# Performance work log

Measured on AMD Instinct MI355X. Metric: run time of the kernel, lower is better.

## Reference

```python
import jax, jax.numpy as jnp
import numpy as np

D_K = 128
D_V = 128
SEQ_LEN = 2048


def setup_inputs() -> dict:
    key = jax.random.key(0)
    kq, kk, kv = jax.random.split(key, 3)
    q = jax.random.normal(kq, (SEQ_LEN, D_K), dtype=jnp.float32)
    k = jax.random.normal(kk, (SEQ_LEN, D_K), dtype=jnp.float32)
    v = jax.random.normal(kv, (SEQ_LEN, D_V), dtype=jnp.float32)
    return {"q": q, "k": k, "v": v}


def _step(carry, qkv):
    J, Svv, Sqv, Sqq, l = carry
    q, k, v = qkv
    l = l + 1
    fl = l.astype(J.dtype)
    # update_correlations: running means of outer products
    Svv = (fl - 1.0) / fl * Svv + jnp.outer(v, v) / fl
    Sqv = (fl - 1.0) / fl * Sqv + jnp.outer(q, v) / fl
    Sqq = (fl - 1.0) / fl * Sqq + jnp.outer(q, q) / fl

    first = l == 1

    # ecological params (J: [d_v, d_k], Sqv: [d_k, d_v], Sqq: [d_k, d_k])
    s_J = jnp.einsum('vk,kv->', J, Sqv)            # trace(J @ Sigma_qv)
    s_l = k @ Sqv @ v
    A_JJ = jnp.einsum('vk,kj,vj->', J, Sqq, J)     # trace(J Sqq J^T)
    A_ll = (v @ v) * (k @ Sqq @ k)
    A_Jl = v @ J @ Sqq @ k

    # safe denominators (unused branches must not produce NaN under where)
    A_JJ_s = jnp.where(first | (A_JJ == 0), 1.0, A_JJ)
    A_ll_s = jnp.where(first | (A_ll == 0), 1.0, A_ll)
    denom = A_JJ * A_ll - A_Jl ** 2
    denom_s = jnp.where(first | (denom == 0), 1.0, denom)

    margin = s_l - A_Jl * (s_J / A_JJ_s)

    wf = (A_ll * s_J - A_Jl * s_l) / denom_s
    wi = (A_JJ * s_l - A_Jl * s_J) / denom_s
    # nonnegativity constraints (check omega_i first, as in the source)
    wf_c = jnp.where(wi <= 0, s_J / A_JJ_s, jnp.where(wf <= 0, 0.0, wf))
    wi_c = jnp.where(wi <= 0, 0.0, jnp.where(wf <= 0, s_l / A_ll_s, wi))

    do_update = margin > 0
    vk = jnp.outer(v, k)
    J_upd = jnp.where(do_update, wf_c * J + wi_c * vk, J)
    J_new = jnp.where(first, vk, J_upd)
    updated = first | do_update

    # compute_cost with updated J and correlations
    cost = (0.5 * jnp.trace(Svv)
            - jnp.einsum('vk,kv->', J_new, Sqv)
            + 0.5 * jnp.einsum('vk,kj,vj->', J_new, Sqq, J_new))

    return (J_new, Svv, Sqv, Sqq, l), (cost, updated)


def _run(q, k, v):
    d_k, d_v = q.shape[-1], v.shape[-1]
    init = (jnp.zeros((d_v, d_k), q.dtype),
            jnp.zeros((d_v, d_v), q.dtype),
            jnp.zeros((d_k, d_v), q.dtype),
            jnp.zeros((d_k, d_k), q.dtype),
            jnp.int32(0))
    (J, _, _, _, _), (costs, updated) = jax.lax.scan(_step, init, (q, k, v))
    return costs, updated, J


def reference(q, k, v):
    return _run(q, k, v)
```

## Files before the change

kernel.cpp:

```cpp
#include <hip/hip_runtime.h>

#define SEQ 2048
#define D 128

__global__ __launch_bounds__(256) void precompute_kernel(
    const float* __restrict__ q, const float* __restrict__ k, const float* __restrict__ v,
    float* __restrict__ U, float* __restrict__ sl, float* __restrict__ kqq,
    float* __restrict__ vv, float* __restrict__ kq_adj, float* __restrict__ vv_adj,
    float* __restrict__ kU_adj, double* __restrict__ invl)
{
    const int s = blockIdx.x;
    const int tid = threadIdx.x;

    __shared__ float ks[D];
    __shared__ float vs[D];
    __shared__ float alpha[SEQ];
    __shared__ float red[8];
    __shared__ float upart[256];

    if (tid < D) ks[tid] = k[s * D + tid];
    else if (tid < 2 * D) vs[tid - D] = v[s * D + (tid - D)];
    __syncthreads();

    float p_a2 = 0.f, p_ab = 0.f;
    for (int i = tid; i <= s; i += 256) {
        const float4* qr = (const float4*)(q + (size_t)i * D);
        const float4* vr = (const float4*)(v + (size_t)i * D);
        float a = 0.f, b = 0.f;
#pragma unroll
        for (int j = 0; j < D / 4; ++j) {
            float4 q4 = qr[j];
            float4 v4 = vr[j];
            a += q4.x * ks[4 * j + 0] + q4.y * ks[4 * j + 1] + q4.z * ks[4 * j + 2] + q4.w * ks[4 * j + 3];
            b += v4.x * vs[4 * j + 0] + v4.y * vs[4 * j + 1] + v4.z * vs[4 * j + 2] + v4.w * vs[4 * j + 3];
        }
        alpha[i] = a;
        p_a2 += a * a;
        p_ab += a * b;
        if (i == s) vv[s] = b;
    }
#pragma unroll
    for (int off = 1; off < 64; off <<= 1) {
        p_a2 += __shfl_xor(p_a2, off);
        p_ab += __shfl_xor(p_ab, off);
    }
    const int wid = tid >> 6;
    if ((tid & 63) == 0) { red[wid] = p_a2; red[4 + wid] = p_ab; }
    __syncthreads();
    if (tid == 0) {
        kqq[s] = red[0] + red[1] + red[2] + red[3];
        sl[s]  = red[4] + red[5] + red[6] + red[7];
        invl[s] = 1.0 / (double)(s + 1);
    }

    if (tid < 64) {
        if (s + 1 < SEQ) {
            float p2 = ks[tid] * q[(size_t)(s + 1) * D + tid]
                     + ks[tid + 64] * q[(size_t)(s + 1) * D + 64 + tid];
#pragma unroll
            for (int off = 1; off < 64; off <<= 1) p2 += __shfl_xor(p2, off);
            if (tid == 0) kq_adj[s + 1] = p2;
        }
        if (s == 0 && tid == 0) { kq_adj[0] = 0.f; kU_adj[0] = 0.f; vv_adj[0] = 0.f; }
    } else if (tid < 128 && s > 0) {
        const int t2 = tid - 64;
        float p2 = vs[t2] * v[(size_t)(s - 1) * D + t2]
                 + vs[t2 + 64] * v[(size_t)(s - 1) * D + 64 + t2];
#pragma unroll
        for (int off = 1; off < 64; off <<= 1) p2 += __shfl_xor(p2, off);
        if (t2 == 0) vv_adj[s] = p2;
    }

    const int c = tid & (D - 1);
    const int h = tid >> 7;
    float a0 = 0.f, a1 = 0.f, a2 = 0.f, a3 = 0.f;
    int i = h;
    for (; i + 6 <= s; i += 8) {
        a0 = fmaf(q[(size_t)(i    ) * D + c], alpha[i    ], a0);
        a1 = fmaf(q[(size_t)(i + 2) * D + c], alpha[i + 2], a1);
        a2 = fmaf(q[(size_t)(i + 4) * D + c], alpha[i + 4], a2);
        a3 = fmaf(q[(size_t)(i + 6) * D + c], alpha[i + 6], a3);
    }
    for (; i <= s; i += 2) a0 = fmaf(q[(size_t)i * D + c], alpha[i], a0);
    upart[tid] = (a0 + a1) + (a2 + a3);
    __syncthreads();

    float kup = 0.f;
    if (tid < D) {
        const float uv = upart[tid] + upart[tid + D];
        U[(size_t)s * D + tid] = uv;
        if (s > 0) kup = uv * k[(size_t)(s - 1) * D + tid];
    }
#pragma unroll
    for (int off = 1; off < 64; off <<= 1) kup += __shfl_xor(kup, off);
    if (tid == 0)  red[0] = kup;
    if (tid == 64) red[1] = kup;
    __syncthreads();
    if (s > 0 && tid == 0) kU_adj[s] = red[0] + red[1];
}

#define DPP_ADD(x, ctrl) \
    ((x) + __int_as_float(__builtin_amdgcn_update_dpp(0, __float_as_int(x), (ctrl), 0xf, 0xf, true)))
#define COMBINE8(x) do { x = DPP_ADD(x, 0xB1); x = DPP_ADD(x, 0x4E); x = DPP_ADD(x, 0x141); } while (0)
#define TAIL3(x)    do { x = DPP_ADD(x, 0x140); x = DPP_ADD(x, 0x142); x = DPP_ADD(x, 0x143); } while (0)
#define REDUCE16(x) do { x = DPP_ADD(x, 0xB1); x = DPP_ADD(x, 0x4E); x = DPP_ADD(x, 0x141); \
                         x = DPP_ADD(x, 0x140); } while (0)

#define UPDATE_J(MODE, WF, WI)                                                            \
    if ((MODE) == 2) {                                                                    \
        jr0.x = vcur*kk0.x; jr0.y = vcur*kk0.y; jr0.z = vcur*kk0.z; jr0.w = vcur*kk0.w;   \
        jr1.x = vcur*kk1.x; jr1.y = vcur*kk1.y; jr1.z = vcur*kk1.z; jr1.w = vcur*kk1.w;   \
        jr2.x = vcur*kk2.x; jr2.y = vcur*kk2.y; jr2.z = vcur*kk2.z; jr2.w = vcur*kk2.w;   \
        jr3.x = vcur*kk3.x; jr3.y = vcur*kk3.y; jr3.z = vcur*kk3.z; jr3.w = vcur*kk3.w;   \
    } else if ((MODE) == 1) {                                                             \
        const float wvr = (WI) * vcur;                                                    \
        jr0.x = fmaf(jr0.x, (WF), wvr*kk0.x); jr0.y = fmaf(jr0.y, (WF), wvr*kk0.y);       \
        jr0.z = fmaf(jr0.z, (WF), wvr*kk0.z); jr0.w = fmaf(jr0.w, (WF), wvr*kk0.w);       \
        jr1.x = fmaf(jr1.x, (WF), wvr*kk1.x); jr1.y = fmaf(jr1.y, (WF), wvr*kk1.y);       \
        jr1.z = fmaf(jr1.z, (WF), wvr*kk1.z); jr1.w = fmaf(jr1.w, (WF), wvr*kk1.w);       \
        jr2.x = fmaf(jr2.x, (WF), wvr*kk2.x); jr2.y = fmaf(jr2.y, (WF), wvr*kk2.y);       \
        jr2.z = fmaf(jr2.z, (WF), wvr*kk2.z); jr2.w = fmaf(jr2.w, (WF), wvr*kk2.w);       \
        jr3.x = fmaf(jr3.x, (WF), wvr*kk3.x); jr3.y = fmaf(jr3.y, (WF), wvr*kk3.y);       \
        jr3.z = fmaf(jr3.z, (WF), wvr*kk3.z); jr3.w = fmaf(jr3.w, (WF), wvr*kk3.w);       \
    }

__global__ __launch_bounds__(1024, 4) void scan_kernel(
    const float* __restrict__ q, const float* __restrict__ k, const float* __restrict__ v,
    const float* __restrict__ U, const float* __restrict__ sl_arr,
    const float* __restrict__ kqq_arr, const float* __restrict__ vv_arr,
    const float* __restrict__ kq_adj, const float* __restrict__ vv_adj,
    const float* __restrict__ kU_adj, const double* __restrict__ invl_arr,
    float* __restrict__ out)
{
    const int tid  = threadIdx.x;
    const int lane = tid & 63;
    const int w    = __builtin_amdgcn_readfirstlane(tid >> 6);
    const int r    = tid >> 3;
    const int cg   = tid & 7;
    const int c0s  = cg * 20;

    float4 jr0 = make_float4(0.f, 0.f, 0.f, 0.f);
    float4 jr1 = jr0, jr2 = jr0, jr3 = jr0;

    __shared__ float ring[3][3][160];
    __shared__ __align__(16) float wred[2][16][4];
    __shared__ __align__(16) float decLDS[2][4];

    const bool stager = (tid >= 384) && (tid < 768);
    const int  which  = (tid >> 7) - 3;
    const int  sidx   = tid & 127;
    const int  widx   = ((sidx >> 4) * 20) + (sidx & 15);

    float gstage = 0.f;
    if (stager) {
        if (which == 0) {
            ring[0][0][widx] = q[(size_t)1 * D + sidx];
            ring[1][0][widx] = q[(size_t)2 * D + sidx];
            gstage = q[(size_t)3 * D + sidx];
        } else if (which == 1) {
            ring[0][1][widx] = U[(size_t)1 * D + sidx];
            ring[1][1][widx] = U[(size_t)2 * D + sidx];
            gstage = U[(size_t)3 * D + sidx];
        } else {
            ring[0][2][widx] = k[sidx];
            ring[1][2][widx] = k[(size_t)1 * D + sidx];
            gstage = k[(size_t)2 * D + sidx];
        }
    }
    float vcur = v[r], vnext = v[(size_t)D + r], vn2 = v[(size_t)2 * D + r];

    float dwf = 0.f, dwi = 1.f;
    int dmode = 2;
    if (tid == 0) { decLDS[0][0] = 0.f; decLDS[0][1] = 1.f; decLDS[0][2] = 2.f; decLDS[0][3] = 0.f; }

    double SJ = 0.0, AJJ = 0.0, trSvv = 0.0;
    if (w == 0) {
        const double sl0 = (double)sl_arr[0];
        const double kq0 = (double)kqq_arr[0];
        const double vv0 = (double)vv_arr[0];
        trSvv = vv0;
        SJ  = sl0;
        AJJ = vv0 * kq0;
        if (lane == 0) {
            out[0] = (float)((0.5 * trSvv - SJ + 0.5 * AJJ) * invl_arr[0]);
            out[SEQ] = 1.f;
        }
    }
    __syncthreads();

    for (int i = 0; i < SEQ - 1; ++i) {
        const int p    = i % 3;
        const int pw   = (i + 2) % 3;
        const int par  = i & 1;
        const int parn = (i + 1) & 1;

        float c_sl = 0.f, c_kq = 0.f, c_vv = 0.f, c_kqa = 0.f, c_vva = 0.f,
              c_vvp = 0.f, c_kua = 0.f;
        double c_inv = 0.0;
        if (w == 0) {
            c_sl  = sl_arr[i + 1];  c_kq  = kqq_arr[i + 1]; c_vv  = vv_arr[i + 1];
            c_kqa = kq_adj[i + 1];  c_vva = vv_adj[i + 1];  c_vvp = vv_arr[i];
            c_kua = kU_adj[i + 1];  c_inv = invl_arr[i + 1];
        }

        const float4* q4 = (const float4*)&ring[p][0][c0s];
        const float4* u4 = (const float4*)&ring[p][1][c0s];
        const float4* k4 = (const float4*)&ring[p][2][c0s];
        const float4 qa = q4[0], qb = q4[1], qc = q4[2], qd = q4[3];
        const float4 ua = u4[0], ub = u4[1], uc = u4[2], ud = u4[3];
        const float4 kk0 = k4[0], kk1 = k4[1], kk2 = k4[2], kk3 = k4[3];

        float pa = jr0.x * qa.x, pb = jr2.x * qc.x;
        pa = fmaf(jr0.y, qa.y, pa); pb = fmaf(jr2.y, qc.y, pb);
        pa = fmaf(jr0.z, qa.z, pa); pb = fmaf(jr2.z, qc.z, pb);
        pa = fmaf(jr0.w, qa.w, pa); pb = fmaf(jr2.w, qc.w, pb);
        pa = fmaf(jr1.x, qb.x, pa); pb = fmaf(jr3.x, qd.x, pb);
        pa = fmaf(jr1.y, qb.y, pa); pb = fmaf(jr3.y, qd.y, pb);
        pa = fmaf(jr1.z, qb.z, pa); pb = fmaf(jr3.z, qd.z, pb);
        pa = fmaf(jr1.w, qb.w, pa); pb = fmaf(jr3.w, qd.w, pb);
        float Yq = pa + pb;
        float va_ = jr0.x * ua.x, vb_ = jr2.x * uc.x;
        va_ = fmaf(jr0.y, ua.y, va_); vb_ = fmaf(jr2.y, uc.y, vb_);
        va_ = fmaf(jr0.z, ua.z, va_); vb_ = fmaf(jr2.z, uc.z, vb_);
        va_ = fmaf(jr0.w, ua.w, va_); vb_ = fmaf(jr2.w, uc.w, vb_);
        va_ = fmaf(jr1.x, ub.x, va_); vb_ = fmaf(jr3.x, ud.x, vb_);
        va_ = fmaf(jr1.y, ub.y, va_); vb_ = fmaf(jr3.y, ud.y, vb_);
        va_ = fmaf(jr1.z, ub.z, va_); vb_ = fmaf(jr3.z, ud.z, vb_);
        va_ = fmaf(jr1.w, ub.w, va_); vb_ = fmaf(jr3.w, ud.w, vb_);
        float Yw = va_ + vb_;

        COMBINE8(Yq);
        COMBINE8(Yw);
        float z1 = vnext * Yq;
        float z2 = Yq * Yq;
        float z3 = vcur  * Yq;
        float z4 = vnext * Yw;
        TAIL3(z1);
        TAIL3(z2);
        TAIL3(z3);
        TAIL3(z4);
        if (lane == 63) *(float4*)&wred[par][w][0] = make_float4(z1, z2, z3, z4);

        if (stager) {
            ring[pw][which][widx] = gstage;
            const int tq = (i + 4 < SEQ) ? i + 4 : SEQ - 1;
            const int tk = (i + 3 < SEQ) ? i + 3 : SEQ - 1;
            gstage = (which == 0) ? q[(size_t)tq * D + sidx]
                   : (which == 1) ? U[(size_t)tq * D + sidx]
                                  : k[(size_t)tk * D + sidx];
        }
        const int tv = (i + 3 < SEQ) ? i + 3 : SEQ - 1;
        const float vnew = v[(size_t)tv * D + r];

        __syncthreads();

        if (w == 0) {
            float4 ww = *(const float4*)&wred[par][lane & 15][0];
            const float odwf = dwf, odwi = dwi;
            const int   odmode = dmode;
            UPDATE_J(odmode, odwf, odwi)

            REDUCE16(ww.x);
            REDUCE16(ww.y);
            REDUCE16(ww.z);
            REDUCE16(ww.w);

            double a, b;
            if (odmode == 2)      { a = 0.0; b = 1.0; }
            else if (odmode == 1) { a = (double)odwf; b = (double)odwi; }
            else                  { a = 1.0; b = 0.0; }
            const double kqa = (double)c_kqa, vva = (double)c_vva;
            const double vvp = (double)c_vvp, kua = (double)c_kua;
            const double r1 = (double)ww.x * 0.125, r2 = (double)ww.y * 0.125;
            const double r3 = (double)ww.z * 0.125, r4 = (double)ww.w * 0.125;
            const double Jqv  = a * r1 + b * (kqa * vva);
            const double Jq2  = a * a * r2 + 2.0 * a * b * kqa * r3 + b * b * kqa * kqa * vvp;
            const double AJl_ = a * r4 + b * kua * vva;

            trSvv += (double)c_vv;
            SJ    += Jqv;
            AJJ   += Jq2;
            const double s_l  = (double)c_sl;
            const double A_ll = (double)c_vv * (double)c_kq;
            const double AJJ_s  = (AJJ == 0.0)  ? 1.0 : AJJ;
            const double A_ll_s = (A_ll == 0.0) ? 1.0 : A_ll;
            const double denom   = AJJ * A_ll - AJl_ * AJl_;
            const double denom_s = (denom == 0.0) ? 1.0 : denom;
            const double rden = 1.0 / denom_s;
            const double wf = (A_ll * SJ - AJl_ * s_l) * rden;
            const double wi = (AJJ * s_l - AJl_ * SJ) * rden;
            double wf_c, wi_c;
            if (wi <= 0.0)      { wf_c = SJ / AJJ_s;  wi_c = 0.0; }
            else if (wf <= 0.0) { wf_c = 0.0;         wi_c = s_l / A_ll_s; }
            else                { wf_c = wf;          wi_c = wi; }
            const bool do_update = (s_l * AJJ_s - AJl_ * SJ) > 0.0;

            int mode;
            if (do_update) {
                mode = 1;
                const double nSJ = wf_c * SJ + wi_c * s_l;
                AJJ = wf_c * wf_c * AJJ + 2.0 * wf_c * wi_c * AJl_ + wi_c * wi_c * A_ll;
                SJ = nSJ;
            } else {
                mode = 0;
            }

            dwf = (float)wf_c; dwi = (float)wi_c; dmode = mode;
            if (lane == 0) {
                out[i + 1] = (float)((0.5 * trSvv - SJ + 0.5 * AJJ) * c_inv);
                out[SEQ + i + 1] = mode ? 1.f : 0.f;
                *(float4*)&decLDS[parn][0] = make_float4(dwf, dwi, (float)mode, 0.f);
            }
        } else {
            const float4 df = *(const float4*)&decLDS[par][0];
            dwf = df.x; dwi = df.y; dmode = (int)df.z;
            UPDATE_J(dmode, dwf, dwi)
        }

        vcur = vnext; vnext = vn2; vn2 = vnew;
    }

    __syncthreads();
    {
        const float4 df = *(const float4*)&decLDS[(SEQ - 1) & 1][0];
        const float fwf = df.x, fwi = df.y;
        const int   fmode = (int)df.z;
        const int p = (SEQ - 1) % 3;
        const float4* k4 = (const float4*)&ring[p][2][c0s];
        const float4 kk0 = k4[0], kk1 = k4[1], kk2 = k4[2], kk3 = k4[3];
        UPDATE_J(fmode, fwf, fwi)
        float* jbase = out + 2 * SEQ + (size_t)r * D + cg * 16;
        *(float4*)(jbase + 0)  = jr0;
        *(float4*)(jbase + 4)  = jr1;
        *(float4*)(jbase + 8)  = jr2;
        *(float4*)(jbase + 12) = jr3;
    }
}

extern "C" void kernel_launch(void* const* d_in, const int* in_sizes, int n_in,
                              void* d_out, int out_size, void* d_ws, size_t ws_size,
                              hipStream_t stream) {
    (void)in_sizes; (void)n_in; (void)out_size; (void)ws_size;
    const float* q = (const float*)d_in[0];
    const float* k = (const float*)d_in[1];
    const float* v = (const float*)d_in[2];
    float* out = (float*)d_out;

    float* U      = (float*)d_ws;
    float* sl     = U + (size_t)SEQ * D;
    float* kqq    = sl + SEQ;
    float* vv     = kqq + SEQ;
    float* kq_adj = vv + SEQ;
    float* vv_adj = kq_adj + SEQ;
    float* kU_adj = vv_adj + SEQ;
    double* invl  = (double*)(kU_adj + SEQ);

    precompute_kernel<<<SEQ, 256, 0, stream>>>(q, k, v, U, sl, kqq, vv,
                                               kq_adj, vv_adj, kU_adj, invl);
    scan_kernel<<<1, 1024, 0, stream>>>(q, k, v, U, sl, kqq, vv,
                                        kq_adj, vv_adj, kU_adj, invl, out);
}
```

Baseline: 2.657 ms.

## Deepen prefetch of staged rows and per-step scalars, split dot-product chains

The stager threads now keep two rows in registers instead of one, so global loads for q/U/k are issued one iteration further ahead. Wave 0 loads the per-step scalar coefficients one iteration early and rotates them, which takes global-load latency off the serial decision path. The dot-product FMA chains are split into four independent accumulators instead of two to shorten dependency chains. The cost is extra register pressure, and the summation order changes slightly.

```diff
diff --git a/kernel.cpp b/kernel.cpp
--- a/kernel.cpp
+++ b/kernel.cpp
@@ -151,20 +151,23 @@
     const int  sidx   = tid & 127;
     const int  widx   = ((sidx >> 4) * 20) + (sidx & 15);
 
-    float gstage = 0.f;
+    float g0 = 0.f, g1 = 0.f;
     if (stager) {
         if (which == 0) {
             ring[0][0][widx] = q[(size_t)1 * D + sidx];
             ring[1][0][widx] = q[(size_t)2 * D + sidx];
-            gstage = q[(size_t)3 * D + sidx];
+            g0 = q[(size_t)3 * D + sidx];
+            g1 = q[(size_t)4 * D + sidx];
         } else if (which == 1) {
             ring[0][1][widx] = U[(size_t)1 * D + sidx];
             ring[1][1][widx] = U[(size_t)2 * D + sidx];
-            gstage = U[(size_t)3 * D + sidx];
+            g0 = U[(size_t)3 * D + sidx];
+            g1 = U[(size_t)4 * D + sidx];
         } else {
             ring[0][2][widx] = k[sidx];
             ring[1][2][widx] = k[(size_t)1 * D + sidx];
-            gstage = k[(size_t)2 * D + sidx];
+            g0 = k[(size_t)2 * D + sidx];
+            g1 = k[(size_t)3 * D + sidx];
         }
     }
     float vcur = v[r], vnext = v[(size_t)D + r], vn2 = v[(size_t)2 * D + r];
@@ -174,6 +177,9 @@
     if (tid == 0) { decLDS[0][0] = 0.f; decLDS[0][1] = 1.f; decLDS[0][2] = 2.f; decLDS[0][3] = 0.f; }
 
     double SJ = 0.0, AJJ = 0.0, trSvv = 0.0;
+    float  csl = 0.f, ckq = 0.f, cvv = 0.f, ckqa = 0.f, cvva = 0.f,
+           cvvp = 0.f, ckua = 0.f;
+    double cinv = 0.0;
     if (w == 0) {
         const double sl0 = (double)sl_arr[0];
         const double kq0 = (double)kqq_arr[0];
@@ -185,6 +191,9 @@
             out[0] = (float)((0.5 * trSvv - SJ + 0.5 * AJJ) * invl_arr[0]);
             out[SEQ] = 1.f;
         }
+        csl  = sl_arr[1];  ckq  = kqq_arr[1]; cvv  = vv_arr[1];
+        ckqa = kq_adj[1];  cvva = vv_adj[1];  cvvp = vv_arr[0];
+        ckua = kU_adj[1];  cinv = invl_arr[1];
     }
     __syncthreads();
 
@@ -192,15 +201,16 @@
         const int p    = i % 3;
         const int pw   = (i + 2) % 3;
         const int par  = i & 1;
-        const int parn = (i + 1) & 1;
-
-        float c_sl = 0.f, c_kq = 0.f, c_vv = 0.f, c_kqa = 0.f, c_vva = 0.f,
-              c_vvp = 0.f, c_kua = 0.f;
-        double c_inv = 0.0;
+        const int parn = 1 - par;
+
+        float nsl = 0.f, nkq = 0.f, nvv = 0.f, nkqa = 0.f, nvva = 0.f,
+              nvvp = 0.f, nkua = 0.f;
+        double ninv = 0.0;
         if (w == 0) {
-            c_sl  = sl_arr[i + 1];  c_kq  = kqq_arr[i + 1]; c_vv  = vv_arr[i + 1];
-            c_kqa = kq_adj[i + 1];  c_vva = vv_adj[i + 1];  c_vvp = vv_arr[i];
-            c_kua = kU_adj[i + 1];  c_inv = invl_arr[i + 1];
+            const int t2 = (i + 2 < SEQ) ? i + 2 : SEQ - 1;
+            nsl  = sl_arr[t2];  nkq  = kqq_arr[t2]; nvv  = vv_arr[t2];
+            nkqa = kq_adj[t2];  nvva = vv_adj[t2];  nvvp = vv_arr[i + 1];
+            nkua = kU_adj[t2];  ninv = invl_arr[t2];
         }
 
         const float4* q4 = (const float4*)&ring[p][0][c0s];
@@ -210,24 +220,22 @@
         const float4 ua = u4[0], ub = u4[1], uc = u4[2], ud = u4[3];
         const float4 kk0 = k4[0], kk1 = k4[1], kk2 = k4[2], kk3 = k4[3];
 
-        float pa = jr0.x * qa.x, pb = jr2.x * qc.x;
-        pa = fmaf(jr0.y, qa.y, pa); pb = fmaf(jr2.y, qc.y, pb);
-        pa = fmaf(jr0.z, qa.z, pa); pb = fmaf(jr2.z, qc.z, pb);
-        pa = fmaf(jr0.w, qa.w, pa); pb = fmaf(jr2.w, qc.w, pb);
-        pa = fmaf(jr1.x, qb.x, pa); pb = fmaf(jr3.x, qd.x, pb);
-        pa = fmaf(jr1.y, qb.y, pa); pb = fmaf(jr3.y, qd.y, pb);
-        pa = fmaf(jr1.z, qb.z, pa); pb = fmaf(jr3.z, qd.z, pb);
-        pa = fmaf(jr1.w, qb.w, pa); pb = fmaf(jr3.w, qd.w, pb);
-        float Yq = pa + pb;
-        float va_ = jr0.x * ua.x, vb_ = jr2.x * uc.x;
-        va_ = fmaf(jr0.y, ua.y, va_); vb_ = fmaf(jr2.y, uc.y, vb_);
-        va_ = fmaf(jr0.z, ua.z, va_); vb_ = fmaf(jr2.z, uc.z, vb_);
-        va_ = fmaf(jr0.w, ua.w, va_); vb_ = fmaf(jr2.w, uc.w, vb_);
-        va_ = fmaf(jr1.x, ub.x, va_); vb_ = fmaf(jr3.x, ud.x, vb_);
-        va_ = fmaf(jr1.y, ub.y, va_); vb_ = fmaf(jr3.y, ud.y, vb_);
-        va_ = fmaf(jr1.z, ub.z, va_); vb_ = fmaf(jr3.z, ud.z, vb_);
-        va_ = fmaf(jr1.w, ub.w, va_); vb_ = fmaf(jr3.w, ud.w, vb_);
-        float Yw = va_ + vb_;
+        float p0 = jr0.x * qa.x, p1 = jr1.x * qb.x, p2 = jr2.x * qc.x, p3 = jr3.x * qd.x;
+        p0 = fmaf(jr0.y, qa.y, p0); p1 = fmaf(jr1.y, qb.y, p1);
+        p2 = fmaf(jr2.y, qc.y, p2); p3 = fmaf(jr3.y, qd.y, p3);
+        p0 = fmaf(jr0.z, qa.z, p0); p1 = fmaf(jr1.z, qb.z, p1);
+        p2 = fmaf(jr2.z, qc.z, p2); p3 = fmaf(jr3.z, qd.z, p3);
+        p0 = fmaf(jr0.w, qa.w, p0); p1 = fmaf(jr1.w, qb.w, p1);
+        p2 = fmaf(jr2.w, qc.w, p2); p3 = fmaf(jr3.w, qd.w, p3);
+        float Yq = (p0 + p1) + (p2 + p3);
+        float s0 = jr0.x * ua.x, s1 = jr1.x * ub.x, s2 = jr2.x * uc.x, s3 = jr3.x * ud.x;
+        s0 = fmaf(jr0.y, ua.y, s0); s1 = fmaf(jr1.y, ub.y, s1);
+        s2 = fmaf(jr2.y, uc.y, s2); s3 = fmaf(jr3.y, ud.y, s3);
+        s0 = fmaf(jr0.z, ua.z, s0); s1 = fmaf(jr1.z, ub.z, s1);
+        s2 = fmaf(jr2.z, uc.z, s2); s3 = fmaf(jr3.z, ud.z, s3);
+        s0 = fmaf(jr0.w, ua.w, s0); s1 = fmaf(jr1.w, ub.w, s1);
+        s2 = fmaf(jr2.w, uc.w, s2); s3 = fmaf(jr3.w, ud.w, s3);
+        float Yw = (s0 + s1) + (s2 + s3);
 
         COMBINE8(Yq);
         COMBINE8(Yw);
@@ -242,12 +250,13 @@
         if (lane == 63) *(float4*)&wred[par][w][0] = make_float4(z1, z2, z3, z4);
 
         if (stager) {
-            ring[pw][which][widx] = gstage;
-            const int tq = (i + 4 < SEQ) ? i + 4 : SEQ - 1;
-            const int tk = (i + 3 < SEQ) ? i + 3 : SEQ - 1;
-            gstage = (which == 0) ? q[(size_t)tq * D + sidx]
-                   : (which == 1) ? U[(size_t)tq * D + sidx]
-                                  : k[(size_t)tk * D + sidx];
+            ring[pw][which][widx] = g0;
+            g0 = g1;
+            const int tq = (i + 5 < SEQ) ? i + 5 : SEQ - 1;
+            const int tk = (i + 4 < SEQ) ? i + 4 : SEQ - 1;
+            g1 = (which == 0) ? q[(size_t)tq * D + sidx]
+               : (which == 1) ? U[(size_t)tq * D + sidx]
+                              : k[(size_t)tk * D + sidx];
         }
         const int tv = (i + 3 < SEQ) ? i + 3 : SEQ - 1;
         const float vnew = v[(size_t)tv * D + r];
@@ -269,19 +278,19 @@
             if (odmode == 2)      { a = 0.0; b = 1.0; }
             else if (odmode == 1) { a = (double)odwf; b = (double)odwi; }
             else                  { a = 1.0; b = 0.0; }
-            const double kqa = (double)c_kqa, vva = (double)c_vva;
-            const double vvp = (double)c_vvp, kua = (double)c_kua;
+            const double kqa = (double)ckqa, vva = (double)cvva;
+            const double vvp = (double)cvvp, kua = (double)ckua;
             const double r1 = (double)ww.x * 0.125, r2 = (double)ww.y * 0.125;
             const double r3 = (double)ww.z * 0.125, r4 = (double)ww.w * 0.125;
             const double Jqv  = a * r1 + b * (kqa * vva);
             const double Jq2  = a * a * r2 + 2.0 * a * b * kqa * r3 + b * b * kqa * kqa * vvp;
             const double AJl_ = a * r4 + b * kua * vva;
 
-            trSvv += (double)c_vv;
+            trSvv += (double)cvv;
             SJ    += Jqv;
             AJJ   += Jq2;
-            const double s_l  = (double)c_sl;
-            const double A_ll = (double)c_vv * (double)c_kq;
+            const double s_l  = (double)csl;
+            const double A_ll = (double)cvv * (double)ckq;
             const double AJJ_s  = (AJJ == 0.0)  ? 1.0 : AJJ;
             const double A_ll_s = (A_ll == 0.0) ? 1.0 : A_ll;
             const double denom   = AJJ * A_ll - AJl_ * AJl_;
@@ -307,10 +316,12 @@
 
             dwf = (float)wf_c; dwi = (float)wi_c; dmode = mode;
             if (lane == 0) {
-                out[i + 1] = (float)((0.5 * trSvv - SJ + 0.5 * AJJ) * c_inv);
+                out[i + 1] = (float)((0.5 * trSvv - SJ + 0.5 * AJJ) * cinv);
                 out[SEQ + i + 1] = mode ? 1.f : 0.f;
                 *(float4*)&decLDS[parn][0] = make_float4(dwf, dwi, (float)mode, 0.f);
             }
+            csl = nsl; ckq = nkq; cvv = nvv; ckqa = nkqa; cvva = nvva;
+            cvvp = nvvp; ckua = nkua; cinv = ninv;
         } else {
             const float4 df = *(const float4*)&decLDS[par][0];
             dwf = df.x; dwi = df.y; dmode = (int)df.z;
```

Result: slower. 3.120 ms (+17.4%).
